# Performance work log

Hardware: AMD Instinct MI355X
Metric: run time of the kernel (lower is better)

Reference implementation:

```python
import jax, jax.numpy as jnp
import numpy as np

KEY_DIM, VALUE_DIM, N_ACTIONS = 128, 64, 256
B, L = 32, 2048


def setup_inputs() -> dict:
    key = jax.random.key(0)
    k1, k2, k3 = jax.random.split(key, 3)
    key_vectors = jax.random.normal(k1, (B, L, KEY_DIM), dtype=jnp.float32)
    value_vectors = jax.random.normal(k2, (B, N_ACTIONS, KEY_DIM), dtype=jnp.float32)
    weights = jax.random.normal(k3, (KEY_DIM, VALUE_DIM, N_ACTIONS), dtype=jnp.float32)
    return {"key_vectors": key_vectors, "value_vectors": value_vectors, "weights": weights}


def reference(key_vectors, value_vectors, weights):
    # torch: einsum('bln,nka->bla', key, W) sums over both n (key_dim) and k (value_dim)
    scores = jnp.einsum('bln,nka->bla', key_vectors, weights)  # (B, L, A)
    # fused multiply-then-reduce over actions == batched matmul (no (B,L,A,D) intermediate)
    mem_vectors = jnp.einsum('bla,bad->bld', scores, value_vectors)  # (B, L, key_dim)
    q_values = jnp.einsum('bln,bmn->blm', key_vectors, mem_vectors)  # (B, L, L)
    return q_values
```

## Files before the change

kernel.cpp:

```cpp
#include <hip/hip_runtime.h>
#include <hip/hip_bf16.h>

#define KD 128
#define VD 64
#define NA 256
#define NB 32
#define LL 2048

typedef __attribute__((ext_vector_type(8))) short bf16x8;
typedef __attribute__((ext_vector_type(4))) float f32x4;
typedef __attribute__((ext_vector_type(8))) unsigned short u16x8;
typedef __attribute__((ext_vector_type(4))) unsigned short u16x4;

static __device__ __forceinline__ unsigned short f2bf(float x) {
  __hip_bfloat16 h = __float2bfloat16(x);
  unsigned short u;
  __builtin_memcpy(&u, &h, 2);
  return u;
}

__global__ __launch_bounds__(256) void fold_w(const float* __restrict__ W,
                                              float* __restrict__ W2) {
  const int idx = blockIdx.x * 256 + threadIdx.x;
  const int n = idx >> 8, a = idx & 255;
  const float* p = W + (long)n * (VD * NA) + a;
  float s = 0.f;
  #pragma unroll
  for (int k = 0; k < VD; ++k) s += p[k * NA];
  W2[idx] = s;
}

__global__ __launch_bounds__(128) void compute_t(const float* __restrict__ W2,
                                                 const float* __restrict__ V,
                                                 unsigned short* __restrict__ Tt) {
  const int n = threadIdx.x;
  const int d0 = blockIdx.x * 8;
  const int b = blockIdx.y;
  const float* vb = V + (long)b * NA * KD + d0;
  const float* w2p = W2 + n * NA;
  float acc[8] = {0.f, 0.f, 0.f, 0.f, 0.f, 0.f, 0.f, 0.f};
  for (int a = 0; a < NA; a += 4) {
    const float4 w = *(const float4*)(w2p + a);
    const float wq[4] = {w.x, w.y, w.z, w.w};
    #pragma unroll
    for (int q = 0; q < 4; ++q) {
      const float* vr = vb + (long)(a + q) * KD;
      #pragma unroll
      for (int j = 0; j < 8; ++j) acc[j] += wq[q] * vr[j];
    }
  }
  #pragma unroll
  for (int j = 0; j < 8; ++j)
    Tt[((long)b * KD + d0 + j) * KD + n] = f2bf(acc[j]);
}

__global__ __launch_bounds__(256) void cvt_key(const float* __restrict__ in,
                                               unsigned short* __restrict__ out) {
  const long i = ((long)blockIdx.x * 256 + threadIdx.x) * 8;
  const float4 f0 = *(const float4*)(in + i);
  const float4 f1 = *(const float4*)(in + i + 4);
  u16x8 r;
  r[0] = f2bf(f0.x); r[1] = f2bf(f0.y); r[2] = f2bf(f0.z); r[3] = f2bf(f0.w);
  r[4] = f2bf(f1.x); r[5] = f2bf(f1.y); r[6] = f2bf(f1.z); r[7] = f2bf(f1.w);
  *(u16x8*)(out + i) = r;
}

template <bool OUTBF16>
__global__ __launch_bounds__(256) void gemm_nt(const unsigned short* __restrict__ A,
                                               const unsigned short* __restrict__ Bm,
                                               void* __restrict__ Cv,
                                               int Bn, int nNT) {
  __shared__ unsigned short lds[32768];

  const int nper = gridDim.x >> 3;
  const int lg = (blockIdx.x & 7) * nper + (blockIdx.x >> 3);
  const int nt = lg % nNT;
  const int rest = lg / nNT;
  const int mt = rest & 15;
  const int b = rest >> 4;

  const int tid = threadIdx.x;
  const int lane = tid & 63, w = tid >> 6;
  const int l15 = lane & 15, lhi = lane >> 4;

  const unsigned short* gA = A + ((long)b * LL + mt * 128) * KD;
  const unsigned short* gB = Bm + ((long)b * Bn + nt * 128) * KD;

  unsigned short* ldsA = lds;
  unsigned short* ldsB = lds + 16384;

  #pragma unroll
  for (int i = 0; i < 8; ++i) {
    const int addr = (w * 8 + i) * 1024 + lane * 16;
    const int row = addr >> 8;
    const int src = addr ^ ((row & 7) << 4);
    __builtin_amdgcn_global_load_lds(
        (const __attribute__((address_space(1))) void*)((const char*)gA + src),
        (__attribute__((address_space(3))) void*)((char*)ldsA + addr), 16, 0, 0);
    __builtin_amdgcn_global_load_lds(
        (const __attribute__((address_space(1))) void*)((const char*)gB + src),
        (__attribute__((address_space(3))) void*)((char*)ldsB + addr), 16, 0, 0);
  }
  __syncthreads();

  const int wr = w >> 1, wc = w & 1;
  f32x4 acc[4][4];
  #pragma unroll
  for (int i = 0; i < 4; ++i)
    #pragma unroll
    for (int j = 0; j < 4; ++j) acc[i][j] = f32x4{0.f, 0.f, 0.f, 0.f};

  #pragma unroll
  for (int ks = 0; ks < 4; ++ks) {
    const int kb = (ks * 32 + lhi * 8) * 2;
    bf16x8 av[4], bv[4];
    #pragma unroll
    for (int mf = 0; mf < 4; ++mf) {
      const int row = wr * 64 + mf * 16 + l15;
      const int byte = (row * 256 + kb) ^ ((row & 7) << 4);
      av[mf] = *(const bf16x8*)((const char*)ldsA + byte);
    }
    #pragma unroll
    for (int nf = 0; nf < 4; ++nf) {
      const int row = wc * 64 + nf * 16 + l15;
      const int byte = (row * 256 + kb) ^ ((row & 7) << 4);
      bv[nf] = *(const bf16x8*)((const char*)ldsB + byte);
    }
    #pragma unroll
    for (int mf = 0; mf < 4; ++mf)
      #pragma unroll
      for (int nf = 0; nf < 4; ++nf)
        acc[mf][nf] = __builtin_amdgcn_mfma_f32_16x16x32_bf16(bv[nf], av[mf],
                                                              acc[mf][nf], 0, 0, 0);
  }

  const long row0 = (long)b * LL + mt * 128 + wr * 64;
  const int col0 = nt * 128 + wc * 64;
  if (OUTBF16) {
    unsigned short* C = (unsigned short*)Cv;
    #pragma unroll
    for (int mf = 0; mf < 4; ++mf)
      #pragma unroll
      for (int nf = 0; nf < 4; ++nf) {
        const long r = row0 + mf * 16 + l15;
        const int c = col0 + nf * 16 + lhi * 4;
        u16x4 v;
        #pragma unroll
        for (int i = 0; i < 4; ++i) v[i] = f2bf(acc[mf][nf][i]);
        *(u16x4*)(C + r * Bn + c) = v;
      }
  } else {
    float* C = (float*)Cv;
    #pragma unroll
    for (int mf = 0; mf < 4; ++mf)
      #pragma unroll
      for (int nf = 0; nf < 4; ++nf) {
        const long r = row0 + mf * 16 + l15;
        const int c = col0 + nf * 16 + lhi * 4;
        *(f32x4*)(C + r * Bn + c) = acc[mf][nf];
      }
  }
}

extern "C" void kernel_launch(void* const* d_in, const int* in_sizes, int n_in,
                              void* d_out, int out_size, void* d_ws, size_t ws_size,
                              hipStream_t stream) {
  const float* key = (const float*)d_in[0];
  const float* val = (const float*)d_in[1];
  const float* wts = (const float*)d_in[2];
  float* out = (float*)d_out;

  char* ws = (char*)d_ws;
  float* W2 = (float*)ws;
  unsigned short* Tt = (unsigned short*)(ws + 131072);
  unsigned short* keyB = (unsigned short*)(ws + 131072 + 1048576);
  unsigned short* memB = (unsigned short*)(ws + 131072 + 1048576 + 16777216);

  fold_w<<<128, 256, 0, stream>>>(wts, W2);
  compute_t<<<dim3(16, NB), 128, 0, stream>>>(W2, val, Tt);
  cvt_key<<<4096, 256, 0, stream>>>(key, keyB);
  gemm_nt<true><<<16 * NB, 256, 0, stream>>>(keyB, Tt, memB, KD, 1);
  gemm_nt<false><<<16 * 16 * NB, 256, 0, stream>>>(keyB, memB, out, LL, 16);
}
```

Before: 191.0 us.

## Make Q GEMM persistent over N tiles with double-buffered LDS staging

The final key·mem^T GEMM now launches one block per (batch, M tile) instead of one per output tile. Each block keeps its A fragments in registers and loops over the 16 N tiles, prefetching the next B tile into the alternate LDS buffer while computing the current one. This removes the repeated A loads and per-block launch and prologue costs, and overlaps global-to-LDS transfer with MFMA work. In exchange the grid shrinks to 512 blocks, and register pressure rises from holding all A fragments.

```diff
diff --git a/kernel.cpp b/kernel.cpp
--- a/kernel.cpp
+++ b/kernel.cpp
@@ -17,6 +17,12 @@
   unsigned short u;
   __builtin_memcpy(&u, &h, 2);
   return u;
+}
+
+static __device__ __forceinline__ void stage16(const void* gsrc, void* ldst) {
+  __builtin_amdgcn_global_load_lds(
+      (const __attribute__((address_space(1))) void*)gsrc,
+      (__attribute__((address_space(3))) void*)ldst, 16, 0, 0);
 }
 
 __global__ __launch_bounds__(256) void fold_w(const float* __restrict__ W,
@@ -65,26 +71,21 @@
   *(u16x8*)(out + i) = r;
 }
 
-template <bool OUTBF16>
-__global__ __launch_bounds__(256) void gemm_nt(const unsigned short* __restrict__ A,
-                                               const unsigned short* __restrict__ Bm,
-                                               void* __restrict__ Cv,
-                                               int Bn, int nNT) {
+__global__ __launch_bounds__(256) void gemm_mem(const unsigned short* __restrict__ A,
+                                                const unsigned short* __restrict__ Bm,
+                                                unsigned short* __restrict__ C) {
   __shared__ unsigned short lds[32768];
-
   const int nper = gridDim.x >> 3;
   const int lg = (blockIdx.x & 7) * nper + (blockIdx.x >> 3);
-  const int nt = lg % nNT;
-  const int rest = lg / nNT;
-  const int mt = rest & 15;
-  const int b = rest >> 4;
+  const int mt = lg & 15;
+  const int b = lg >> 4;
 
   const int tid = threadIdx.x;
   const int lane = tid & 63, w = tid >> 6;
   const int l15 = lane & 15, lhi = lane >> 4;
 
   const unsigned short* gA = A + ((long)b * LL + mt * 128) * KD;
-  const unsigned short* gB = Bm + ((long)b * Bn + nt * 128) * KD;
+  const unsigned short* gB = Bm + (long)b * KD * KD;
 
   unsigned short* ldsA = lds;
   unsigned short* ldsB = lds + 16384;
@@ -94,12 +95,8 @@
     const int addr = (w * 8 + i) * 1024 + lane * 16;
     const int row = addr >> 8;
     const int src = addr ^ ((row & 7) << 4);
-    __builtin_amdgcn_global_load_lds(
-        (const __attribute__((address_space(1))) void*)((const char*)gA + src),
-        (__attribute__((address_space(3))) void*)((char*)ldsA + addr), 16, 0, 0);
-    __builtin_amdgcn_global_load_lds(
-        (const __attribute__((address_space(1))) void*)((const char*)gB + src),
-        (__attribute__((address_space(3))) void*)((char*)ldsB + addr), 16, 0, 0);
+    stage16((const char*)gA + src, (char*)ldsA + addr);
+    stage16((const char*)gB + src, (char*)ldsB + addr);
   }
   __syncthreads();
 
@@ -135,30 +132,121 @@
   }
 
   const long row0 = (long)b * LL + mt * 128 + wr * 64;
-  const int col0 = nt * 128 + wc * 64;
-  if (OUTBF16) {
-    unsigned short* C = (unsigned short*)Cv;
+  const int col0 = wc * 64;
+  #pragma unroll
+  for (int mf = 0; mf < 4; ++mf)
+    #pragma unroll
+    for (int nf = 0; nf < 4; ++nf) {
+      const long r = row0 + mf * 16 + l15;
+      const int c = col0 + nf * 16 + lhi * 4;
+      u16x4 v;
+      #pragma unroll
+      for (int i = 0; i < 4; ++i) v[i] = f2bf(acc[mf][nf][i]);
+      *(u16x4*)(C + r * KD + c) = v;
+    }
+}
+
+__global__ __launch_bounds__(256) void gemm_q(const unsigned short* __restrict__ A,
+                                              const unsigned short* __restrict__ Bm,
+                                              float* __restrict__ C) {
+  __shared__ unsigned short lds[32768];
+  const int lg = (blockIdx.x & 7) * 64 + (blockIdx.x >> 3);
+  const int b = lg >> 4, mt = lg & 15;
+
+  const int tid = threadIdx.x;
+  const int lane = tid & 63, w = tid >> 6;
+  const int l15 = lane & 15, lhi = lane >> 4;
+  const int wr = w >> 1, wc = w & 1;
+
+  const unsigned short* gA = A + ((long)b * LL + mt * 128) * KD;
+  const unsigned short* gBp = Bm + (long)b * LL * KD;
+
+  unsigned short* buf0 = lds;
+  unsigned short* buf1 = lds + 16384;
+
+  #pragma unroll
+  for (int i = 0; i < 8; ++i) {
+    const int addr = (w * 8 + i) * 1024 + lane * 16;
+    const int row = addr >> 8;
+    const int src = addr ^ ((row & 7) << 4);
+    stage16((const char*)gA + src, (char*)buf0 + addr);
+    stage16((const char*)gBp + src, (char*)buf1 + addr);
+  }
+  asm volatile("s_waitcnt vmcnt(0)" ::: "memory");
+  __builtin_amdgcn_s_barrier();
+  __builtin_amdgcn_sched_barrier(0);
+
+  bf16x8 af[4][4];
+  #pragma unroll
+  for (int ks = 0; ks < 4; ++ks) {
+    const int kb = (ks * 32 + lhi * 8) * 2;
+    #pragma unroll
+    for (int mf = 0; mf < 4; ++mf) {
+      const int row = wr * 64 + mf * 16 + l15;
+      const int byte = (row * 256 + kb) ^ ((row & 7) << 4);
+      af[ks][mf] = *(const bf16x8*)((const char*)buf0 + byte);
+    }
+  }
+  asm volatile("s_waitcnt lgkmcnt(0)" ::: "memory");
+  __builtin_amdgcn_s_barrier();
+  __builtin_amdgcn_sched_barrier(0);
+
+  const long row0 = (long)b * LL + mt * 128 + wr * 64;
+
+  #pragma unroll 2
+  for (int ntile = 0; ntile < 16; ++ntile) {
+    unsigned short* cbuf = (ntile & 1) ? buf0 : buf1;
+    unsigned short* sbuf = (ntile & 1) ? buf1 : buf0;
+
+    if (ntile < 15) {
+      const char* gB = (const char*)(gBp + (long)(ntile + 1) * 128 * KD);
+      #pragma unroll
+      for (int i = 0; i < 8; ++i) {
+        const int addr = (w * 8 + i) * 1024 + lane * 16;
+        const int row = addr >> 8;
+        const int src = addr ^ ((row & 7) << 4);
+        stage16(gB + src, (char*)sbuf + addr);
+      }
+    }
+    __builtin_amdgcn_sched_barrier(0);
+
+    f32x4 acc[4][4];
+    #pragma unroll
+    for (int i = 0; i < 4; ++i)
+      #pragma unroll
+      for (int j = 0; j < 4; ++j) acc[i][j] = f32x4{0.f, 0.f, 0.f, 0.f};
+
+    #pragma unroll
+    for (int ks = 0; ks < 4; ++ks) {
+      const int kb = (ks * 32 + lhi * 8) * 2;
+      bf16x8 bv[4];
+      #pragma unroll
+      for (int nf = 0; nf < 4; ++nf) {
+        const int row = wc * 64 + nf * 16 + l15;
+        const int byte = (row * 256 + kb) ^ ((row & 7) << 4);
+        bv[nf] = *(const bf16x8*)((const char*)cbuf + byte);
+      }
+      #pragma unroll
+      for (int mf = 0; mf < 4; ++mf)
+        #pragma unroll
+        for (int nf = 0; nf < 4; ++nf)
+          acc[mf][nf] = __builtin_amdgcn_mfma_f32_16x16x32_bf16(bv[nf], af[ks][mf],
+                                                                acc[mf][nf], 0, 0, 0);
+    }
+
+    const int col0 = ntile * 128 + wc * 64;
     #pragma unroll
     for (int mf = 0; mf < 4; ++mf)
       #pragma unroll
       for (int nf = 0; nf < 4; ++nf) {
         const long r = row0 + mf * 16 + l15;
         const int c = col0 + nf * 16 + lhi * 4;
-        u16x4 v;
-        #pragma unroll
-        for (int i = 0; i < 4; ++i) v[i] = f2bf(acc[mf][nf][i]);
-        *(u16x4*)(C + r * Bn + c) = v;
+        *(f32x4*)(C + r * LL + c) = acc[mf][nf];
       }
-  } else {
-    float* C = (float*)Cv;
-    #pragma unroll
-    for (int mf = 0; mf < 4; ++mf)
-      #pragma unroll
-      for (int nf = 0; nf < 4; ++nf) {
-        const long r = row0 + mf * 16 + l15;
-        const int c = col0 + nf * 16 + lhi * 4;
-        *(f32x4*)(C + r * Bn + c) = acc[mf][nf];
-      }
+
+    asm volatile("s_waitcnt vmcnt(16)" ::: "memory");
+    __builtin_amdgcn_s_barrier();
+    __builtin_amdgcn_sched_barrier(0);
   }
 }
 
@@ -179,6 +267,6 @@
   fold_w<<<128, 256, 0, stream>>>(wts, W2);
   compute_t<<<dim3(16, NB), 128, 0, stream>>>(W2, val, Tt);
   cvt_key<<<4096, 256, 0, stream>>>(key, keyB);
-  gemm_nt<true><<<16 * NB, 256, 0, stream>>>(keyB, Tt, memB, KD, 1);
-  gemm_nt<false><<<16 * 16 * NB, 256, 0, stream>>>(keyB, memB, out, LL, 16);
-}
+  gemm_mem<<<16 * NB, 256, 0, stream>>>(keyB, Tt, memB);
+  gemm_q<<<16 * NB, 256, 0, stream>>>(keyB, memB, out);
+}
```

Measured after the change: 208.6 us. +9.2%, slower.
